# Performance work log

Hardware: AMD Instinct MI355X
Metric: run time of the kernel (lower is better)

The kernel has to match this reference:

```python
import jax, jax.numpy as jnp
import numpy as np

DT = jnp.float32(0.001)
A = (0.0, 0.5, 0.5, 1.0)  # RK4 stage coefficients from the source


def _rbf(y1, centers, gammas, weights):
    # Gaussian RBF: sum_k w_k * exp(-((y - c_k) * gamma_k)^2); y1: [B] -> [B]
    phi = jnp.exp(-jnp.square((y1[:, None] - centers[None, :]) * gammas[None, :]))  # [B,K]
    return phi @ weights  # [B]


def _fun(u, y1, centers, gammas, weights):
    # Faithful to _fun: returns [[ydot], [(u - 214.9261*ydot - 19.3607*sign(ydot) - rbf(ydot) + 3.2902)/95.45]]
    acc = (u - y1 * 214.9261 - 19.3607 * jnp.sign(y1) - _rbf(y1, centers, gammas, weights) + 3.2902) / 95.45
    return jnp.stack([y1, acc], axis=-1)  # [B,2]


def setup_inputs() -> dict:
    key = jax.random.key(0)
    k1, k2, k3, k4, k5 = jax.random.split(key, 5)
    B, K = 1048576, 128
    return {
        "inputs": jax.random.normal(k1, (B,), dtype=jnp.float32),
        "states": jax.random.normal(k2, (B, 2), dtype=jnp.float32),
        "rbf_centers": jax.random.normal(k3, (K,), dtype=jnp.float32),
        "rbf_gammas": jax.random.uniform(k4, (K,), dtype=jnp.float32),
        "rbf_weights": jax.random.normal(k5, (K,), dtype=jnp.float32),
    }


def reference(inputs, states, rbf_centers, rbf_gammas, rbf_weights):
    # ydot = states.view(2,-1) -> per-sample state [B,2]; only ydot[1] feeds _fun
    y1 = states[:, 1]  # [B] velocity component
    yddoti = _fun(inputs, y1, rbf_centers, rbf_gammas, rbf_weights)  # [B,2]
    dy1 = yddoti[:, 1] * DT  # only component 1 of the offset state is used by _fun
    # NOTE (faithful bug): all stage offsets use yddoti, not the previous k.
    k1 = _fun(inputs, y1 + A[0] * dy1, rbf_centers, rbf_gammas, rbf_weights)
    k2 = _fun(inputs, y1 + A[1] * dy1, rbf_centers, rbf_gammas, rbf_weights)
    k3 = _fun(inputs, y1 + A[2] * dy1, rbf_centers, rbf_gammas, rbf_weights)
    k4 = _fun(inputs, y1 + A[3] * dy1, rbf_centers, rbf_gammas, rbf_weights)
    # NOTE (faithful): source returns dt/6*(k1+2k2+2k3+k4) WITHOUT adding the old state.
    st_n = (DT / 6.0) * (k1 + 2.0 * k2 + 2.0 * k3 + k4)  # [B,2]
    return st_n
```

## Files before the change

### kernel.cpp

```cpp
#include <hip/hip_runtime.h>

#define KCENT 128
#define BLOCK 256
#define TN    512
#define YMIN  (-9.0f)
#define YMAX  (9.0f)

#if __has_builtin(__builtin_amdgcn_exp2f)
#define EXP2F(x) __builtin_amdgcn_exp2f(x)
#else
#define EXP2F(x) exp2f(x)
#endif


__global__ __launch_bounds__(256) void build_table_kernel(
    const float* __restrict__ centers,
    const float* __restrict__ gammas,
    const float* __restrict__ weights,
    float4* __restrict__ tab)
{
    const int gid  = blockIdx.x * blockDim.x + threadIdx.x;
    const int node = gid >> 6;
    const int lane = gid & 63;
    if (node >= TN) return;
    const float SQRT_LOG2E = 1.2011224087864498f;
    const float TWO_LN2    = 1.3862943611198906f;
    const float h  = (YMAX - YMIN) / (float)(TN - 1);
    const float y0 = YMIN + node * h;
    const float y1 = y0 + h;
    float F0 = 0.f, P0 = 0.f, F1 = 0.f, P1 = 0.f;
    #pragma unroll
    for (int kk = 0; kk < KCENT / 64; ++kk) {
        const int k = lane + kk * 64;
        float g  = gammas[k];
        float w  = weights[k];
        float a  = g * SQRT_LOG2E;
        float b  = a * centers[k];
        float w2 = -TWO_LN2 * a * w;
        float x0 = __builtin_fmaf(a, y0, -b);
        float p0 = EXP2F(-(x0 * x0));
        F0 = __builtin_fmaf(w, p0, F0);
        P0 = __builtin_fmaf(w2, x0 * p0, P0);
        float x1 = __builtin_fmaf(a, y1, -b);
        float p1 = EXP2F(-(x1 * x1));
        F1 = __builtin_fmaf(w, p1, F1);
        P1 = __builtin_fmaf(w2, x1 * p1, P1);
    }
    #pragma unroll
    for (int off = 32; off > 0; off >>= 1) {
        F0 += __shfl_xor(F0, off);
        P0 += __shfl_xor(P0, off);
        F1 += __shfl_xor(F1, off);
        P1 += __shfl_xor(P1, off);
    }
    if (lane == 0) tab[node] = make_float4(F0, P0, F1 - F0, P1 - P0);
}

__device__ __forceinline__ float2 rk4_elem(float u, float yy,
                                           const float4* sT, float INVH) {
    float tpos = (yy - YMIN) * INVH;
    int idx = (int)tpos;
    idx = idx < 0 ? 0 : (idx > TN - 2 ? TN - 2 : idx);
    float fr = tpos - (float)idx;
    float4 n = sT[idx];
    float F  = __builtin_fmaf(fr, n.z, n.x);
    float Fp = __builtin_fmaf(fr, n.w, n.y);

    const float INV95 = 1.0f / 95.45f;
    float s1 = (yy > 0.f) ? 1.f : ((yy < 0.f) ? -1.f : 0.f);
    float a1 = (u - yy * 214.9261f - 19.3607f * s1 - F + 3.2902f) * INV95;
    float dy = a1 * 0.001f;
    float h2 = 0.5f * dy;
    float y2 = yy + h2;
    float y4 = yy + dy;
    float rb2 = __builtin_fmaf(Fp, h2, F);
    float rb4 = __builtin_fmaf(Fp, dy, F);
    float s2 = (y2 > 0.f) ? 1.f : ((y2 < 0.f) ? -1.f : 0.f);
    float a2 = (u - y2 * 214.9261f - 19.3607f * s2 - rb2 + 3.2902f) * INV95;
    float s4 = (y4 > 0.f) ? 1.f : ((y4 < 0.f) ? -1.f : 0.f);
    float a4 = (u - y4 * 214.9261f - 19.3607f * s4 - rb4 + 3.2902f) * INV95;

    const float DT6 = 0.001f / 6.0f;
    return make_float2(DT6 * (yy + 4.f * y2 + y4),
                       DT6 * (a1 + 4.f * a2 + a4));
}

__global__ __launch_bounds__(BLOCK) void rk4_tab_kernel(
    const float* __restrict__ inputs,
    const float* __restrict__ states,
    const float4* __restrict__ tab,
    float* __restrict__ out, int B, int halfB)
{
    __shared__ float4 sT[TN];

    const int p = blockIdx.x * BLOCK + threadIdx.x;
    const bool valid = p < halfB;

    float2 uu = make_float2(0.f, 0.f);
    float4 ss = make_float4(0.f, 0.f, 0.f, 0.f);
    if (valid) {
        uu = ((const float2*)inputs)[p];
        ss = ((const float4*)states)[p];
    }

    #pragma unroll
    for (int t = threadIdx.x; t < TN; t += BLOCK) sT[t] = tab[t];
    __syncthreads();

    const float INVH = (float)(TN - 1) / (YMAX - YMIN);
    if (valid) {
        float2 ra = rk4_elem(uu.x, ss.y, sT, INVH);
        float2 rb = rk4_elem(uu.y, ss.w, sT, INVH);
        ((float4*)out)[p] = make_float4(ra.x, ra.y, rb.x, rb.y);
    }

    if ((B & 1) && p == 0) {
        const int i = B - 1;
        float2 r = rk4_elem(inputs[i], ((const float2*)states)[i].y, sT, INVH);
        ((float2*)out)[i] = r;
    }
}

extern "C" void kernel_launch(void* const* d_in, const int* in_sizes, int n_in,
                              void* d_out, int out_size, void* d_ws, size_t ws_size,
                              hipStream_t stream) {
    const float* inputs  = (const float*)d_in[0];
    const float* states  = (const float*)d_in[1];
    const float* centers = (const float*)d_in[2];
    const float* gammas  = (const float*)d_in[3];
    const float* weights = (const float*)d_in[4];
    float* out = (float*)d_out;
    float4* tab = (float4*)d_ws;
    const int B = in_sizes[0];

    build_table_kernel<<<(TN * 64 + 255) / 256, 256, 0, stream>>>(
        centers, gammas, weights, tab);

    const int halfB = B >> 1;
    const int grid = (halfB + BLOCK - 1) / BLOCK;
    rk4_tab_kernel<<<grid > 0 ? grid : 1, BLOCK, 0, stream>>>(
        inputs, states, tab, out, B, halfB);
}
```

Baseline: 74.07 us.

## Fuse RBF table build into RK4 kernel with coarse Hermite interpolation

Removes the separate table-building kernel and has every block compute a 64-node table of RBF value and derivative into shared memory. Lookups switch from linear interpolation on a 512-node table to cubic Hermite interpolation on the coarser table. This drops a kernel launch and the global table round trip. In exchange, each block redundantly evaluates RBF sums, and the coarser grid can cost accuracy.

New measurement: 91.15 us. +23.1%, slower.

```diff
diff --git a/kernel.cpp b/kernel.cpp
--- a/kernel.cpp
+++ b/kernel.cpp
@@ -2,7 +2,7 @@
 
 #define KCENT 128
 #define BLOCK 256
-#define TN    512
+#define TN    64
 #define YMIN  (-9.0f)
 #define YMAX  (9.0f)
 
@@ -13,58 +13,23 @@
 #endif
 
 
-__global__ __launch_bounds__(256) void build_table_kernel(
-    const float* __restrict__ centers,
-    const float* __restrict__ gammas,
-    const float* __restrict__ weights,
-    float4* __restrict__ tab)
-{
-    const int gid  = blockIdx.x * blockDim.x + threadIdx.x;
-    const int node = gid >> 6;
-    const int lane = gid & 63;
-    if (node >= TN) return;
-    const float SQRT_LOG2E = 1.2011224087864498f;
-    const float TWO_LN2    = 1.3862943611198906f;
-    const float h  = (YMAX - YMIN) / (float)(TN - 1);
-    const float y0 = YMIN + node * h;
-    const float y1 = y0 + h;
-    float F0 = 0.f, P0 = 0.f, F1 = 0.f, P1 = 0.f;
-    #pragma unroll
-    for (int kk = 0; kk < KCENT / 64; ++kk) {
-        const int k = lane + kk * 64;
-        float g  = gammas[k];
-        float w  = weights[k];
-        float a  = g * SQRT_LOG2E;
-        float b  = a * centers[k];
-        float w2 = -TWO_LN2 * a * w;
-        float x0 = __builtin_fmaf(a, y0, -b);
-        float p0 = EXP2F(-(x0 * x0));
-        F0 = __builtin_fmaf(w, p0, F0);
-        P0 = __builtin_fmaf(w2, x0 * p0, P0);
-        float x1 = __builtin_fmaf(a, y1, -b);
-        float p1 = EXP2F(-(x1 * x1));
-        F1 = __builtin_fmaf(w, p1, F1);
-        P1 = __builtin_fmaf(w2, x1 * p1, P1);
-    }
-    #pragma unroll
-    for (int off = 32; off > 0; off >>= 1) {
-        F0 += __shfl_xor(F0, off);
-        P0 += __shfl_xor(P0, off);
-        F1 += __shfl_xor(F1, off);
-        P1 += __shfl_xor(P1, off);
-    }
-    if (lane == 0) tab[node] = make_float4(F0, P0, F1 - F0, P1 - P0);
-}
-
 __device__ __forceinline__ float2 rk4_elem(float u, float yy,
-                                           const float4* sT, float INVH) {
+                                           const float2* sF,
+                                           float INVH, float H) {
     float tpos = (yy - YMIN) * INVH;
     int idx = (int)tpos;
     idx = idx < 0 ? 0 : (idx > TN - 2 ? TN - 2 : idx);
-    float fr = tpos - (float)idx;
-    float4 n = sT[idx];
-    float F  = __builtin_fmaf(fr, n.z, n.x);
-    float Fp = __builtin_fmaf(fr, n.w, n.y);
+    float t = tpos - (float)idx;
+    float2 n0 = sF[idx];
+    float2 n1 = sF[idx + 1];
+    float t2 = t * t, t3 = t2 * t;
+    float h00 = 2.f * t3 - 3.f * t2 + 1.f;
+    float h10 = t3 - 2.f * t2 + t;
+    float h01 = 1.f - h00;
+    float h11 = t3 - t2;
+    float F = h00 * n0.x + h10 * (H * n0.y)
+            + h01 * n1.x + h11 * (H * n1.y);
+    float Fp = __builtin_fmaf(t, n1.y - n0.y, n0.y);
 
     const float INV95 = 1.0f / 95.45f;
     float s1 = (yy > 0.f) ? 1.f : ((yy < 0.f) ? -1.f : 0.f);
@@ -85,15 +50,18 @@
                        DT6 * (a1 + 4.f * a2 + a4));
 }
 
-__global__ __launch_bounds__(BLOCK) void rk4_tab_kernel(
+__global__ __launch_bounds__(BLOCK, 8) void rk4_fused_kernel(
     const float* __restrict__ inputs,
     const float* __restrict__ states,
-    const float4* __restrict__ tab,
+    const float* __restrict__ centers,
+    const float* __restrict__ gammas,
+    const float* __restrict__ weights,
     float* __restrict__ out, int B, int halfB)
 {
-    __shared__ float4 sT[TN];
+    __shared__ float2 sF[TN];
 
-    const int p = blockIdx.x * BLOCK + threadIdx.x;
+    const int tid = threadIdx.x;
+    const int p = blockIdx.x * BLOCK + tid;
     const bool valid = p < halfB;
 
     float2 uu = make_float2(0.f, 0.f);
@@ -103,20 +71,42 @@
         ss = ((const float4*)states)[p];
     }
 
-    #pragma unroll
-    for (int t = threadIdx.x; t < TN; t += BLOCK) sT[t] = tab[t];
+    const float SQRT_LOG2E = 1.2011224087864498f;
+    const float TWO_LN2    = 1.3862943611198906f;
+    const float H    = (YMAX - YMIN) / (float)(TN - 1);
+    const float INVH = 1.0f / H;
+    {
+        const int node = tid >> 2;
+        const int q    = tid & 3;
+        const float yn = YMIN + node * H;
+        float F = 0.f, P = 0.f;
+        #pragma unroll 8
+        for (int j = 0; j < KCENT / 4; ++j) {
+            const int k = q * (KCENT / 4) + j;
+            float g  = gammas[k];
+            float w  = weights[k];
+            float a  = g * SQRT_LOG2E;
+            float b  = a * centers[k];
+            float x  = __builtin_fmaf(a, yn, -b);
+            float ph = EXP2F(-(x * x));
+            F = __builtin_fmaf(w, ph, F);
+            P = __builtin_fmaf(-TWO_LN2 * a * w, x * ph, P);
+        }
+        F += __shfl_xor(F, 1); P += __shfl_xor(P, 1);
+        F += __shfl_xor(F, 2); P += __shfl_xor(P, 2);
+        if (q == 0) sF[node] = make_float2(F, P);
+    }
     __syncthreads();
 
-    const float INVH = (float)(TN - 1) / (YMAX - YMIN);
     if (valid) {
-        float2 ra = rk4_elem(uu.x, ss.y, sT, INVH);
-        float2 rb = rk4_elem(uu.y, ss.w, sT, INVH);
+        float2 ra = rk4_elem(uu.x, ss.y, sF, INVH, H);
+        float2 rb = rk4_elem(uu.y, ss.w, sF, INVH, H);
         ((float4*)out)[p] = make_float4(ra.x, ra.y, rb.x, rb.y);
     }
 
     if ((B & 1) && p == 0) {
         const int i = B - 1;
-        float2 r = rk4_elem(inputs[i], ((const float2*)states)[i].y, sT, INVH);
+        float2 r = rk4_elem(inputs[i], ((const float2*)states)[i].y, sF, INVH, H);
         ((float2*)out)[i] = r;
     }
 }
@@ -130,14 +120,10 @@
     const float* gammas  = (const float*)d_in[3];
     const float* weights = (const float*)d_in[4];
     float* out = (float*)d_out;
-    float4* tab = (float4*)d_ws;
     const int B = in_sizes[0];
-
-    build_table_kernel<<<(TN * 64 + 255) / 256, 256, 0, stream>>>(
-        centers, gammas, weights, tab);
 
     const int halfB = B >> 1;
     const int grid = (halfB + BLOCK - 1) / BLOCK;
-    rk4_tab_kernel<<<grid > 0 ? grid : 1, BLOCK, 0, stream>>>(
-        inputs, states, tab, out, B, halfB);
+    rk4_fused_kernel<<<grid > 0 ? grid : 1, BLOCK, 0, stream>>>(
+        inputs, states, centers, gammas, weights, out, B, halfB);
 }
```
